# Kernel tuning notes

Measured on AMD Instinct MI355X. Metric: run time of the kernel, lower is better.

The kernel has to match this reference:

```python
import jax, jax.numpy as jnp
import numpy as np

TEMPERATURE = 0.07
NORMALIZE = True
NEG_INF = -1e30


def setup_inputs() -> dict:
    key = jax.random.key(0)
    features = jax.random.normal(key, (8192, 512), dtype=jnp.float32)
    return {"features": features}


def reference(features):
    # features: [B, D]
    B = features.shape[0]
    if NORMALIZE:
        norm = jnp.linalg.norm(features, axis=1, keepdims=True)
        features = features / jnp.maximum(norm, 1e-12)
    # [B, B] similarity matrix
    sim = jnp.matmul(features, features.T) / TEMPERATURE

    # default SimCLR labels: arange(B//2) repeated twice -> pair (i, i + B//2)
    half = jnp.arange(B // 2, dtype=jnp.int32)
    labels = jnp.concatenate([half, half])
    eq = labels[None, :] == labels[:, None]          # [B, B]
    diag = jnp.eye(B, dtype=bool)
    mask_pos = eq & ~diag                            # positives per row

    # Original per-row CE: logits = cat(pos_sims, neg_sims) (= all j != i),
    # target index 0 = FIRST positive (lowest column index). Loss_i =
    # logsumexp_{j != i}(sim[i, j]) - sim[i, first_pos_i].
    sim_masked = jnp.where(diag, NEG_INF, sim)
    lse = jax.scipy.special.logsumexp(sim_masked, axis=1)   # [B]

    first_pos = jnp.argmax(mask_pos, axis=1)                 # first True per row
    pos_sim = jnp.take_along_axis(sim, first_pos[:, None], axis=1)[:, 0]

    has_pos = jnp.any(mask_pos, axis=1)
    losses = jnp.where(has_pos, lse - pos_sim, 0.0)
    count = jnp.maximum(jnp.sum(has_pos.astype(jnp.float32)), 1.0)
    return jnp.sum(losses) / count
```

## Files before the change

### kernel.cpp

```cpp
#include <hip/hip_runtime.h>
#include <hip/hip_bf16.h>
#include <stdint.h>

#define BATCH 8192
#define DIM   512
#define TILE  128
#define BK    64
#define NT    (BATCH / TILE)
#define NPAIR (NT * (NT + 1) / 2)

typedef __attribute__((ext_vector_type(8))) short short8;
typedef __attribute__((ext_vector_type(4))) float f32x4;

__device__ __forceinline__ void gld_lds16(const void* g, void* l) {
  __builtin_amdgcn_global_load_lds(
      (__attribute__((address_space(1))) void*)(uintptr_t)g,
      (__attribute__((address_space(3))) void*)(uintptr_t)l,
      16, 0, 0);
}

__global__ __launch_bounds__(256) void normalize_bf16(
    const float* __restrict__ x, __hip_bfloat16* __restrict__ o,
    float* __restrict__ rowsum) {
  const int wv = threadIdx.x >> 6, lane = threadIdx.x & 63;
  const int row = blockIdx.x * 4 + wv;
  if (lane == 0) rowsum[row] = 0.0f;
  const float4* xr = (const float4*)(x + (size_t)row * DIM);
  const float4 v0 = xr[lane];
  const float4 v1 = xr[lane + 64];
  float ss = v0.x * v0.x + v0.y * v0.y + v0.z * v0.z + v0.w * v0.w +
             v1.x * v1.x + v1.y * v1.y + v1.z * v1.z + v1.w * v1.w;
#pragma unroll
  for (int m = 32; m > 0; m >>= 1) ss += __shfl_xor(ss, m, 64);
  const float inv = 1.0f / fmaxf(sqrtf(ss), 1e-12f);
  ushort4 p0, p1;
  p0.x = __bfloat16_as_ushort(__float2bfloat16(v0.x * inv));
  p0.y = __bfloat16_as_ushort(__float2bfloat16(v0.y * inv));
  p0.z = __bfloat16_as_ushort(__float2bfloat16(v0.z * inv));
  p0.w = __bfloat16_as_ushort(__float2bfloat16(v0.w * inv));
  p1.x = __bfloat16_as_ushort(__float2bfloat16(v1.x * inv));
  p1.y = __bfloat16_as_ushort(__float2bfloat16(v1.y * inv));
  p1.z = __bfloat16_as_ushort(__float2bfloat16(v1.z * inv));
  p1.w = __bfloat16_as_ushort(__float2bfloat16(v1.w * inv));
  ushort4* orow = (ushort4*)(o + (size_t)row * DIM);
  orow[lane]      = p0;
  orow[lane + 64] = p1;
}

__global__ __launch_bounds__(256, 4) void sim_lse_kernel(
    const __hip_bfloat16* __restrict__ F, float* __restrict__ rowsum,
    float* __restrict__ possim) {
  __shared__ __hip_bfloat16 smem[2 * TILE * BK];
  __shared__ float rowAcc[TILE];
  __shared__ float colAcc[TILE];

  const int t = blockIdx.x;
  int by = (int)((129.0f - sqrtf(129.0f * 129.0f - 8.0f * (float)t)) * 0.5f);
  if (by > NT - 1) by = NT - 1;
  if (by < 0) by = 0;
  while ((by + 1) * (129 - (by + 1)) / 2 <= t) ++by;
  while (by * (129 - by) / 2 > t) --by;
  const int bx = by + (t - by * (129 - by) / 2);
  const bool diagTile = (bx == by);

  const int rowBase = by * TILE;
  const int colBase = bx * TILE;

  const int tid   = threadIdx.x;
  const int lane  = tid & 63;
  const int wv    = tid >> 6;
  const int waveM = wv >> 1;
  const int waveN = wv & 1;
  const int quad  = lane >> 4;
  const int l15   = lane & 15;

  if (tid < TILE) { rowAcc[tid] = 0.0f; colAcc[tid] = 0.0f; }

  f32x4 acc[4][4] = {};

  const int sb = lane & 7;
  const __hip_bfloat16* gA[4];
  const __hip_bfloat16* gB[4];
  char* ldsA[4];
  char* ldsB[4];
#pragma unroll
  for (int c = 0; c < 4; ++c) {
    const int sRow = wv * 32 + c * 8 + (lane >> 3);
    const int g = sb ^ (sRow & 7);
    gA[c] = F + (size_t)(rowBase + sRow) * DIM + g * 8;
    gB[c] = F + (size_t)(colBase + sRow) * DIM + g * 8;
    ldsA[c] = (char*)smem + (wv * 4 + c) * 1024;
    ldsB[c] = (char*)smem + 16384 + (wv * 4 + c) * 1024;
  }

  int aOff[4], bOff[4];
#pragma unroll
  for (int i = 0; i < 4; ++i) {
    const int Ra = waveM * 64 + i * 16 + l15;
    aOff[i] = Ra * 128 + (quad ^ (Ra & 7)) * 16;
    const int Rb = waveN * 64 + i * 16 + l15;
    bOff[i] = 16384 + Rb * 128 + (quad ^ (Rb & 7)) * 16;
  }
  char* sbase = (char*)smem;

  for (int k0 = 0; k0 < DIM; k0 += BK) {
#pragma unroll
    for (int c = 0; c < 4; ++c) {
      gld_lds16(gA[c] + k0, ldsA[c]);
      gld_lds16(gB[c] + k0, ldsB[c]);
    }
    __syncthreads();

    short8 a[4], b[4];
#pragma unroll
    for (int i = 0; i < 4; ++i) {
      a[i] = *(const short8*)(sbase + aOff[i]);
      b[i] = *(const short8*)(sbase + bOff[i]);
    }
#pragma unroll
    for (int mi = 0; mi < 4; ++mi)
#pragma unroll
      for (int ni = 0; ni < 4; ++ni)
        acc[mi][ni] =
            __builtin_amdgcn_mfma_f32_16x16x32_bf16(a[mi], b[ni], acc[mi][ni], 0, 0, 0);
#pragma unroll
    for (int i = 0; i < 4; ++i) {
      a[i] = *(const short8*)(sbase + (aOff[i] ^ 64));
      b[i] = *(const short8*)(sbase + (bOff[i] ^ 64));
    }
#pragma unroll
    for (int mi = 0; mi < 4; ++mi)
#pragma unroll
      for (int ni = 0; ni < 4; ++ni)
        acc[mi][ni] =
            __builtin_amdgcn_mfma_f32_16x16x32_bf16(a[mi], b[ni], acc[mi][ni], 0, 0, 0);
    __syncthreads();
  }

  const float invT = 1.0f / 0.07f;
  float colpart[4] = {0.0f, 0.0f, 0.0f, 0.0f};
#pragma unroll
  for (int mi = 0; mi < 4; ++mi) {
#pragma unroll
    for (int r = 0; r < 4; ++r) {
      const int lrow = waveM * 64 + mi * 16 + quad * 4 + r;
      const int gi = rowBase + lrow;
      const int pj = (gi + 4096) & 8191;
      float rsum = 0.0f;
#pragma unroll
      for (int ni = 0; ni < 4; ++ni) {
        const int gj = colBase + waveN * 64 + ni * 16 + l15;
        const float s = acc[mi][ni][r] * invT;
        if (!diagTile && gj == pj) { possim[gi] = s; possim[gj] = s; }
        const float e = (gi == gj) ? 0.0f : __expf(s);
        rsum += e;
        colpart[ni] += e;
      }
#pragma unroll
      for (int m = 1; m < 16; m <<= 1) rsum += __shfl_xor(rsum, m, 64);
      if (l15 == 0) atomicAdd(&rowAcc[lrow], rsum);
    }
  }
  if (!diagTile) {
#pragma unroll
    for (int ni = 0; ni < 4; ++ni) {
      float c = colpart[ni];
      c += __shfl_xor(c, 16, 64);
      c += __shfl_xor(c, 32, 64);
      if (quad == 0) atomicAdd(&colAcc[waveN * 64 + ni * 16 + l15], c);
    }
  }
  __syncthreads();
  if (tid < TILE) {
    atomicAdd(&rowsum[rowBase + tid], rowAcc[tid]);
    if (!diagTile) atomicAdd(&rowsum[colBase + tid], colAcc[tid]);
  }
}

__global__ __launch_bounds__(256) void finalize_kernel(
    const float* __restrict__ rowsum, const float* __restrict__ possim,
    float* __restrict__ out) {
  float acc = 0.0f;
  for (int i = threadIdx.x; i < BATCH; i += 256)
    acc += logf(rowsum[i]) - possim[i];
#pragma unroll
  for (int m = 32; m > 0; m >>= 1) acc += __shfl_xor(acc, m, 64);
  __shared__ float ws[4];
  const int lane = threadIdx.x & 63, wv = threadIdx.x >> 6;
  if (lane == 0) ws[wv] = acc;
  __syncthreads();
  if (threadIdx.x == 0)
    out[0] = (ws[0] + ws[1] + ws[2] + ws[3]) * (1.0f / (float)BATCH);
}

extern "C" void kernel_launch(void* const* d_in, const int* in_sizes, int n_in,
                              void* d_out, int out_size, void* d_ws, size_t ws_size,
                              hipStream_t stream) {
  const float* x = (const float*)d_in[0];
  float* out = (float*)d_out;

  __hip_bfloat16* Fb = (__hip_bfloat16*)d_ws;
  float* rowsum = (float*)((char*)d_ws + (size_t)BATCH * DIM * sizeof(__hip_bfloat16));
  float* possim = rowsum + BATCH;

  normalize_bf16<<<BATCH / 4, 256, 0, stream>>>(x, Fb, rowsum);
  sim_lse_kernel<<<NPAIR, 256, 0, stream>>>(Fb, rowsum, possim);
  finalize_kernel<<<1, 256, 0, stream>>>(rowsum, possim, out);
}
```

Baseline: 126.4 us.

## Fold temperature into features, use exp2, remap blocks across XCDs, widen finalize

Scales normalized features by sqrt(log2(e)/T) so MFMA outputs are directly base-2 logits, replacing a multiply plus __expf with exp2f and rescaling by ln2 in finalize. Remaps block indices so consecutive tiles land on the same XCD for L2 locality. Splits the epilogue into diagonal and off-diagonal paths, writing positive sims only in the single tile column that holds pairs. Widens the finalize kernel to 1024 threads with fast log. Scaling before the bf16 cast changes rounding slightly.

Measured after the change: 130.0 us. +2.9%, slower.

```diff
diff --git a/kernel.cpp b/kernel.cpp
--- a/kernel.cpp
+++ b/kernel.cpp
@@ -8,6 +8,10 @@
 #define BK    64
 #define NT    (BATCH / TILE)
 #define NPAIR (NT * (NT + 1) / 2)
+#define NXCD  8
+
+#define FEAT_SCALE 4.5398164f
+#define LN2        0.69314718055994531f
 
 typedef __attribute__((ext_vector_type(8))) short short8;
 typedef __attribute__((ext_vector_type(4))) float f32x4;
@@ -32,7 +36,7 @@
              v1.x * v1.x + v1.y * v1.y + v1.z * v1.z + v1.w * v1.w;
 #pragma unroll
   for (int m = 32; m > 0; m >>= 1) ss += __shfl_xor(ss, m, 64);
-  const float inv = 1.0f / fmaxf(sqrtf(ss), 1e-12f);
+  const float inv = FEAT_SCALE / fmaxf(sqrtf(ss), 1e-12f);
   ushort4 p0, p1;
   p0.x = __bfloat16_as_ushort(__float2bfloat16(v0.x * inv));
   p0.y = __bfloat16_as_ushort(__float2bfloat16(v0.y * inv));
@@ -54,7 +58,8 @@
   __shared__ float rowAcc[TILE];
   __shared__ float colAcc[TILE];
 
-  const int t = blockIdx.x;
+  const int t = (blockIdx.x % NXCD) * (NPAIR / NXCD) + blockIdx.x / NXCD;
+
   int by = (int)((129.0f - sqrtf(129.0f * 129.0f - 8.0f * (float)t)) * 0.5f);
   if (by > NT - 1) by = NT - 1;
   if (by < 0) by = 0;
@@ -137,31 +142,52 @@
     __syncthreads();
   }
 
-  const float invT = 1.0f / 0.07f;
-  float colpart[4] = {0.0f, 0.0f, 0.0f, 0.0f};
-#pragma unroll
-  for (int mi = 0; mi < 4; ++mi) {
-#pragma unroll
-    for (int r = 0; r < 4; ++r) {
-      const int lrow = waveM * 64 + mi * 16 + quad * 4 + r;
-      const int gi = rowBase + lrow;
-      const int pj = (gi + 4096) & 8191;
-      float rsum = 0.0f;
-#pragma unroll
-      for (int ni = 0; ni < 4; ++ni) {
-        const int gj = colBase + waveN * 64 + ni * 16 + l15;
-        const float s = acc[mi][ni][r] * invT;
-        if (!diagTile && gj == pj) { possim[gi] = s; possim[gj] = s; }
-        const float e = (gi == gj) ? 0.0f : __expf(s);
-        rsum += e;
-        colpart[ni] += e;
+  if (diagTile) {
+#pragma unroll
+    for (int mi = 0; mi < 4; ++mi) {
+#pragma unroll
+      for (int r = 0; r < 4; ++r) {
+        const int lrow = waveM * 64 + mi * 16 + quad * 4 + r;
+        float rsum = 0.0f;
+#pragma unroll
+        for (int ni = 0; ni < 4; ++ni) {
+          const int lcol = waveN * 64 + ni * 16 + l15;
+          rsum += (lcol == lrow) ? 0.0f : exp2f(acc[mi][ni][r]);
+        }
+#pragma unroll
+        for (int m = 1; m < 16; m <<= 1) rsum += __shfl_xor(rsum, m, 64);
+        if (l15 == 0) atomicAdd(&rowAcc[lrow], rsum);
       }
-#pragma unroll
-      for (int m = 1; m < 16; m <<= 1) rsum += __shfl_xor(rsum, m, 64);
-      if (l15 == 0) atomicAdd(&rowAcc[lrow], rsum);
-    }
-  }
-  if (!diagTile) {
+    }
+  } else {
+    const bool hasPos = (bx == by + 32);
+    float colpart[4] = {0.0f, 0.0f, 0.0f, 0.0f};
+#pragma unroll
+    for (int mi = 0; mi < 4; ++mi) {
+#pragma unroll
+      for (int r = 0; r < 4; ++r) {
+        const int lrow = waveM * 64 + mi * 16 + quad * 4 + r;
+        float rsum = 0.0f;
+#pragma unroll
+        for (int ni = 0; ni < 4; ++ni) {
+          const float s = acc[mi][ni][r];
+          const float e = exp2f(s);
+          rsum += e;
+          colpart[ni] += e;
+          if (hasPos) {
+            const int lcol = waveN * 64 + ni * 16 + l15;
+            if (lcol == lrow) {
+              const int gi = rowBase + lrow;
+              possim[gi] = s;
+              possim[gi + 4096] = s;
+            }
+          }
+        }
+#pragma unroll
+        for (int m = 1; m < 16; m <<= 1) rsum += __shfl_xor(rsum, m, 64);
+        if (l15 == 0) atomicAdd(&rowAcc[lrow], rsum);
+      }
+    }
 #pragma unroll
     for (int ni = 0; ni < 4; ++ni) {
       float c = colpart[ni];
@@ -177,20 +203,24 @@
   }
 }
 
-__global__ __launch_bounds__(256) void finalize_kernel(
+__global__ __launch_bounds__(1024) void finalize_kernel(
     const float* __restrict__ rowsum, const float* __restrict__ possim,
     float* __restrict__ out) {
   float acc = 0.0f;
-  for (int i = threadIdx.x; i < BATCH; i += 256)
-    acc += logf(rowsum[i]) - possim[i];
+  for (int i = threadIdx.x; i < BATCH; i += 1024)
+    acc += __logf(rowsum[i]) - possim[i] * LN2;
 #pragma unroll
   for (int m = 32; m > 0; m >>= 1) acc += __shfl_xor(acc, m, 64);
-  __shared__ float ws[4];
+  __shared__ float ws[16];
   const int lane = threadIdx.x & 63, wv = threadIdx.x >> 6;
   if (lane == 0) ws[wv] = acc;
   __syncthreads();
-  if (threadIdx.x == 0)
-    out[0] = (ws[0] + ws[1] + ws[2] + ws[3]) * (1.0f / (float)BATCH);
+  if (threadIdx.x == 0) {
+    float tot = 0.0f;
+#pragma unroll
+    for (int k = 0; k < 16; ++k) tot += ws[k];
+    out[0] = tot * (1.0f / (float)BATCH);
+  }
 }
 
 extern "C" void kernel_launch(void* const* d_in, const int* in_sizes, int n_in,
@@ -205,5 +235,5 @@
 
   normalize_bf16<<<BATCH / 4, 256, 0, stream>>>(x, Fb, rowsum);
   sim_lse_kernel<<<NPAIR, 256, 0, stream>>>(Fb, rowsum, possim);
-  finalize_kernel<<<1, 256, 0, stream>>>(rowsum, possim, out);
-}
+  finalize_kernel<<<1, 1024, 0, stream>>>(rowsum, possim, out);
+}
```
